# Optimization experiments

Hardware: AMD Instinct MI355X
Metric: run time of the kernel (lower is better)

The kernel has to match this reference:

```python
import jax, jax.numpy as jnp
import numpy as np

B, S, HID = 2, 2048, 2048
H, HKV, HD = 16, 4, 128  # heads, kv heads, head_dim; n_rep = H // HKV


def rotate_half(x):
    h = x.shape[-1] // 2
    return jnp.concatenate((-x[..., h:], x[..., :h]), axis=-1)


def setup_inputs() -> dict:
    key = jax.random.key(0)
    ks = jax.random.split(key, 7)
    sc = 0.02
    return {
        "x": jax.random.normal(ks[0], (B, S, HID), jnp.float32),
        "cos": jax.random.uniform(ks[1], (S, HD), jnp.float32),
        "sin": jax.random.uniform(ks[2], (S, HD), jnp.float32),
        "wq": jax.random.normal(ks[3], (H * HD, HID), jnp.float32) * sc,
        "wk": jax.random.normal(ks[4], (HKV * HD, HID), jnp.float32) * sc,
        "wv": jax.random.normal(ks[5], (HKV * HD, HID), jnp.float32) * sc,
        "wo": jax.random.normal(ks[6], (HID, H * HD), jnp.float32) * sc,
    }


def reference(x, cos, sin, wq, wk, wv, wo):
    bs, seq_len, _ = x.shape
    n_rep = H // HKV

    # projections (Linear with weight [out, in]: y = x @ W.T)
    q = (x @ wq.T).reshape(bs, seq_len, H, HD)
    k = (x @ wk.T).reshape(bs, seq_len, HKV, HD)
    v = (x @ wv.T).reshape(bs, seq_len, HKV, HD)

    # RoPE: cos/sin [S, HD] -> broadcast over heads (unsqueeze_dim=1 after seq)
    c = cos[:seq_len][:, None, :]  # [S,1,HD]
    s = sin[:seq_len][:, None, :]
    q = q * c + rotate_half(q) * s
    k = k * c + rotate_half(k) * s

    # repeat KV heads (GQA) and move heads forward: [b,h,s,d]
    k = jnp.repeat(k, n_rep, axis=2).transpose(0, 2, 1, 3)
    v = jnp.repeat(v, n_rep, axis=2).transpose(0, 2, 1, 3)
    q = q.transpose(0, 2, 1, 3)

    # causal SDPA
    scale = 1.0 / jnp.sqrt(jnp.float32(HD))
    scores = jnp.einsum("bhqd,bhkd->bhqk", q, k) * scale
    causal = jnp.tril(jnp.ones((seq_len, seq_len), bool))
    scores = jnp.where(causal, scores, jnp.float32(-jnp.inf))
    probs = jax.nn.softmax(scores, axis=-1)
    out = jnp.einsum("bhqk,bhkd->bhqd", probs, v)

    out = out.transpose(0, 2, 1, 3).reshape(bs, seq_len, H * HD)
    return out @ wo.T
```

## Files before the change

kernel.cpp:

```cpp
#include <hip/hip_runtime.h>
#include <hip/hip_bf16.h>
#include <math.h>

#define B_    2
#define S_    2048
#define HID_  2048
#define H_    16
#define HKV_  4
#define HD_   128
#define BS_   (B_*S_)
#define QSTRIDE 3072
#define L2E 1.4426950408889634f

typedef __attribute__((ext_vector_type(8))) short bf16x8;
typedef __attribute__((ext_vector_type(4))) float f32x4;
typedef __attribute__((ext_vector_type(16))) float f32x16;
typedef unsigned int uint;

typedef __attribute__((address_space(3))) void lds_void;
typedef __attribute__((address_space(1))) const void gbl_cvoid;

__device__ __forceinline__ void load_lds16(const void* g, void* l) {
  __builtin_amdgcn_global_load_lds((gbl_cvoid*)g, (lds_void*)l, 16, 0, 0);
}

__device__ __forceinline__ unsigned short f2bf(float f) {
  uint u = __float_as_uint(f);
  u = (u + 0x7fff + ((u >> 16) & 1)) >> 16;
  return (unsigned short)u;
}
__device__ __forceinline__ float bf2f(unsigned short u) {
  return __uint_as_float(((uint)u) << 16);
}
__device__ __forceinline__ uint cvtpk_bf16(float lo, float hi) {
  uint r;
  asm("v_cvt_pk_bf16_f32 %0, %1, %2" : "=v"(r) : "v"(lo), "v"(hi));
  return r;
}
__device__ __forceinline__ void swap32(uint& a, uint& b) {
  asm("v_permlane32_swap_b32 %0, %1" : "+v"(a), "+v"(b));
}

__global__ __launch_bounds__(256) void cast_f32_bf16(
    const float* __restrict__ src, unsigned short* __restrict__ dst, int n)
{
  int i = (blockIdx.x * 256 + threadIdx.x) * 4;
  if (i < n) {
    float4 v = *(const float4*)(src + i);
    ushort4 o;
    o.x = f2bf(v.x); o.y = f2bf(v.y); o.z = f2bf(v.z); o.w = f2bf(v.w);
    *(ushort4*)(dst + i) = o;
  }
}

template <int WRITE_BF16>
__global__ __launch_bounds__(256) void gemm_nt_bf16(
    const unsigned short* __restrict__ A, const unsigned short* __restrict__ W,
    void* __restrict__ Cv, int M, int N, int K)
{
  __shared__ unsigned short As[128 * 32];
  __shared__ unsigned short Bs[128 * 32];

  const int tid = threadIdx.x;
  const int bm = blockIdx.y * 128, bn = blockIdx.x * 128;
  const int w = tid >> 6, lane = tid & 63;
  const int c_ = lane & 15, g4 = lane >> 4;
  const int wr = (w >> 1) * 64, wc = (w & 1) * 64;

  f32x4 acc[4][4];
#pragma unroll
  for (int i = 0; i < 4; ++i)
#pragma unroll
    for (int j = 0; j < 4; ++j) acc[i][j] = (f32x4){0.f, 0.f, 0.f, 0.f};

  for (int k0 = 0; k0 < K; k0 += 32) {
#pragma unroll
    for (int i = 0; i < 2; ++i) {
      int db = i * 4096 + tid * 16;
      int row = db >> 6;
      int cb = (db & 63) ^ ((row & 3) << 4);
      load_lds16((const char*)(A + (size_t)(bm + row) * K + k0) + cb, (char*)As + db);
      load_lds16((const char*)(W + (size_t)(bn + row) * K + k0) + cb, (char*)Bs + db);
    }
    __syncthreads();

    bf16x8 af[4], bfr[4];
#pragma unroll
    for (int i = 0; i < 4; ++i) {
      int ra = wr + i * 16 + c_;
      af[i] = *(const bf16x8*)((const char*)As + ra * 64 + ((g4 * 16) ^ ((ra & 3) << 4)));
      int rb = wc + i * 16 + c_;
      bfr[i] = *(const bf16x8*)((const char*)Bs + rb * 64 + ((g4 * 16) ^ ((rb & 3) << 4)));
    }
#pragma unroll
    for (int mi = 0; mi < 4; ++mi)
#pragma unroll
      for (int ni = 0; ni < 4; ++ni)
        acc[mi][ni] = __builtin_amdgcn_mfma_f32_16x16x32_bf16(af[mi], bfr[ni], acc[mi][ni], 0, 0, 0);
    __syncthreads();
  }

#pragma unroll
  for (int mi = 0; mi < 4; ++mi) {
#pragma unroll
    for (int r = 0; r < 4; ++r) {
      size_t row = bm + wr + mi * 16 + g4 * 4 + r;
#pragma unroll
      for (int ni = 0; ni < 4; ++ni) {
        size_t col = bn + wc + ni * 16 + c_;
        float v = acc[mi][ni][r];
        if (WRITE_BF16)
          ((unsigned short*)Cv)[row * N + col] = f2bf(v);
        else
          ((float*)Cv)[row * N + col] = v;
      }
    }
  }
}

template <int NH, int LOGNH, int ROWE, int SCALE>
__global__ __launch_bounds__(256) void rope_bf16(
    unsigned short* __restrict__ p, const float* __restrict__ cosb,
    const float* __restrict__ sinb)
{
  int idx = blockIdx.x * 256 + threadIdx.x;
  int d = idx & 63;
  int h = (idx >> 6) & (NH - 1);
  int s = (idx >> (6 + LOGNH)) & (S_ - 1);
  int b = idx >> (6 + LOGNH + 11);

  size_t off = ((size_t)b * S_ + s) * ROWE + h * HD_ + d;
  float x1 = bf2f(p[off]);
  float x2 = bf2f(p[off + 64]);
  float c1 = cosb[s * HD_ + d],      s1 = sinb[s * HD_ + d];
  float c2 = cosb[s * HD_ + d + 64], s2 = sinb[s * HD_ + d + 64];
  float o1 = x1 * c1 - x2 * s1;
  float o2 = x2 * c2 + x1 * s2;
  if (SCALE) { o1 *= 0.08838834764831845f; o2 *= 0.08838834764831845f; }
  p[off]      = f2bf(o1);
  p[off + 64] = f2bf(o2);
}

__global__ __launch_bounds__(256) void attn_fwd_bf16(
    const unsigned short* __restrict__ QKV, unsigned short* __restrict__ O)
{
  __shared__ __align__(16) char lds[65536];

  const int tid = threadIdx.x;
  const int lane = tid & 63;
  const int wq = tid >> 6;
  const int ql = lane & 31;
  const int hi = lane >> 5;

  const int bid = blockIdx.x;
  const int halfg = bid >> 8, rem = bid & 255;
  const int bh = rem >> 3, a2 = rem & 7;
  const int qt = halfg ? (15 - 2 * a2) : (2 * a2);
  const int b = bh >> 4, h = bh & 15, kh = h >> 2;
  const int q0 = qt * 128;
  const int qglob = q0 + wq * 32 + ql;
  const int ktmax_w = (q0 + wq * 32 + 31) >> 6;
  const int ntiles = 2 * qt + 2;

  bf16x8 qf[8];
  {
    const unsigned short* qsrc =
        QKV + ((size_t)(b * S_) + qglob) * QSTRIDE + h * HD_ + hi * 8;
#pragma unroll
    for (int ds = 0; ds < 8; ++ds) qf[ds] = *(const bf16x8*)(qsrc + ds * 16);
  }

  f32x16 acc[4];
#pragma unroll
  for (int dt = 0; dt < 4; ++dt)
#pragma unroll
    for (int r = 0; r < 16; ++r) acc[dt][r] = 0.f;
  float m_ = -3.0e38f, l_ = 0.f;

  const char* Kg = (const char*)(QKV + (size_t)b * S_ * QSTRIDE + 2048 + kh * HD_);
  const unsigned short* Vg = QKV + (size_t)b * S_ * QSTRIDE + 2560 + kh * HD_;

  const int dc = tid & 15;
  const int kq4 = (tid >> 4) * 4;
  bf16x8 vr[4];

#pragma unroll
  for (int p = 0; p < 4; ++p) {
    int db = p * 4096 + tid * 16;
    int row = db >> 8;
    int cb = (db & 255) ^ ((row & 7) << 4);
    load_lds16(Kg + (size_t)row * (QSTRIDE * 2) + cb, lds + db);
  }
  {
    const unsigned short* vs = Vg + (size_t)kq4 * QSTRIDE + dc * 8;
#pragma unroll
    for (int i = 0; i < 4; ++i) vr[i] = *(const bf16x8*)(vs + i * QSTRIDE);
#pragma unroll
    for (int s = 0; s < 8; ++s) {
      int j = (dc + s) & 7;
      int d = dc * 8 + j;
      uint w0 = (uint)(unsigned short)vr[0][j] | ((uint)(unsigned short)vr[1][j] << 16);
      uint w1 = (uint)(unsigned short)vr[2][j] | ((uint)(unsigned short)vr[3][j] << 16);
      *(uint2*)(lds + 32768 + d * 128 + ((kq4 * 2) ^ (j << 4))) = make_uint2(w0, w1);
    }
  }
  __syncthreads();

  for (int kt = 0; kt < ntiles; ++kt) {
    const int cur = kt & 1;
    const bool pf = (kt + 1 < ntiles);

    if (pf) {
#pragma unroll
      for (int p = 0; p < 4; ++p) {
        int db = p * 4096 + tid * 16;
        int row = db >> 8;
        int cb = (db & 255) ^ ((row & 7) << 4);
        load_lds16(Kg + (size_t)((kt + 1) * 64 + row) * (QSTRIDE * 2) + cb,
                   lds + (cur ^ 1) * 16384 + db);
      }
      const unsigned short* vs = Vg + (size_t)((kt + 1) * 64 + kq4) * QSTRIDE + dc * 8;
#pragma unroll
      for (int i = 0; i < 4; ++i) vr[i] = *(const bf16x8*)(vs + i * QSTRIDE);
    }

    if (kt <= ktmax_w) {
      const char* ksc = lds + cur * 16384;
      const char* vtc = lds + 32768 + cur * 16384;
#pragma unroll
      for (int ks2 = 0; ks2 < 2; ++ks2) {
        f32x16 s;
#pragma unroll
        for (int r = 0; r < 16; ++r) s[r] = 0.f;
        const int kk = ks2 * 32 + ql;
        const char* krow = ksc + kk * 256;
        const int ksw = (kk & 7) << 4;
#pragma unroll
        for (int ds = 0; ds < 8; ++ds) {
          bf16x8 kf = *(const bf16x8*)(krow + ((ds * 32 + hi * 16) ^ ksw));
          s = __builtin_amdgcn_mfma_f32_32x32x16_bf16(kf, qf[ds], s, 0, 0, 0);
        }

        if (kt == ktmax_w) {
          const int kb = kt * 64 + ks2 * 32 + 4 * hi;
#pragma unroll
          for (int r = 0; r < 16; ++r) {
            int kg = kb + (r & 3) + 8 * (r >> 2);
            if (kg > qglob) s[r] = -3.0e38f;
          }
        }

        float mx = s[0];
#pragma unroll
        for (int r = 1; r < 16; ++r) mx = fmaxf(mx, s[r]);
        mx = fmaxf(mx, __shfl_xor(mx, 32));
        const bool nd = mx > m_ + 8.f;
        float fr = 1.f;
        if (__any(nd)) {
          float mn = nd ? mx : m_;
          fr = nd ? exp2f((m_ - mn) * L2E) : 1.f;
          m_ = mn;
#pragma unroll
          for (int dt = 0; dt < 4; ++dt)
#pragma unroll
            for (int r = 0; r < 16; ++r) acc[dt][r] *= fr;
        }
        float pr[16];
        float sum = 0.f;
#pragma unroll
        for (int r = 0; r < 16; ++r) {
          pr[r] = exp2f((s[r] - m_) * L2E);
          sum += pr[r];
        }
        sum += __shfl_xor(sum, 32);
        l_ = l_ * fr + sum;

        uint wA0 = cvtpk_bf16(pr[0], pr[1]);
        uint wA1 = cvtpk_bf16(pr[2], pr[3]);
        uint wB0 = cvtpk_bf16(pr[4], pr[5]);
        uint wB1 = cvtpk_bf16(pr[6], pr[7]);
        swap32(wA0, wB0);
        swap32(wA1, wB1);
        uint wC0 = cvtpk_bf16(pr[8], pr[9]);
        uint wC1 = cvtpk_bf16(pr[10], pr[11]);
        uint wD0 = cvtpk_bf16(pr[12], pr[13]);
        uint wD1 = cvtpk_bf16(pr[14], pr[15]);
        swap32(wC0, wD0);
        swap32(wC1, wD1);
        union { uint u[4]; bf16x8 v; } p0, p1;
        p0.u[0] = wA0; p0.u[1] = wA1; p0.u[2] = wB0; p0.u[3] = wB1;
        p1.u[0] = wC0; p1.u[1] = wC1; p1.u[2] = wD0; p1.u[3] = wD1;

#pragma unroll
        for (int dt = 0; dt < 4; ++dt) {
          const int dr = dt * 32 + ql;
          const char* vrow = vtc + dr * 128;
          const int vsw = (dr & 7) << 4;
          bf16x8 v0 = *(const bf16x8*)(vrow + ((ks2 * 64 + hi * 16) ^ vsw));
          acc[dt] = __builtin_amdgcn_mfma_f32_32x32x16_bf16(v0, p0.v, acc[dt], 0, 0, 0);
          bf16x8 v1 = *(const bf16x8*)(vrow + ((ks2 * 64 + 32 + hi * 16) ^ vsw));
          acc[dt] = __builtin_amdgcn_mfma_f32_32x32x16_bf16(v1, p1.v, acc[dt], 0, 0, 0);
        }
      }
    }

    if (pf) {
#pragma unroll
      for (int s = 0; s < 8; ++s) {
        int j = (dc + s) & 7;
        int d = dc * 8 + j;
        uint w0 = (uint)(unsigned short)vr[0][j] | ((uint)(unsigned short)vr[1][j] << 16);
        uint w1 = (uint)(unsigned short)vr[2][j] | ((uint)(unsigned short)vr[3][j] << 16);
        *(uint2*)(lds + 32768 + (cur ^ 1) * 16384 + d * 128 + ((kq4 * 2) ^ (j << 4))) =
            make_uint2(w0, w1);
      }
    }
    __syncthreads();
  }

  {
    const float inv = 1.f / l_;
    char* wsc = lds + wq * 8704;
#pragma unroll
    for (int dt = 0; dt < 4; ++dt) {
#pragma unroll
      for (int i = 0; i < 8; ++i) {
        uint wv = cvtpk_bf16(acc[dt][2 * i] * inv, acc[dt][2 * i + 1] * inv);
        int d = 2 * (i & 1) + 8 * (i >> 1) + 4 * hi + 32 * dt;
        *(uint*)(wsc + ql * 272 + d * 2) = wv;
      }
    }
#pragma unroll
    for (int j = 0; j < 8; ++j) {
      bf16x8 ov = *(const bf16x8*)(wsc + ql * 272 + hi * 128 + j * 16);
      unsigned short* ob = O + ((size_t)(b * S_) + q0 + wq * 32 + ql) * (H_ * HD_) +
                           h * HD_ + hi * 64 + j * 8;
      *(bf16x8*)ob = ov;
    }
  }
}

extern "C" void kernel_launch(void* const* d_in, const int* in_sizes, int n_in,
                              void* d_out, int out_size, void* d_ws, size_t ws_size,
                              hipStream_t stream) {
  const float* x    = (const float*)d_in[0];
  const float* cosb = (const float*)d_in[1];
  const float* sinb = (const float*)d_in[2];
  const float* wq   = (const float*)d_in[3];
  const float* wk   = (const float*)d_in[4];
  const float* wv   = (const float*)d_in[5];
  const float* wo   = (const float*)d_in[6];
  float* out        = (float*)d_out;

  unsigned short* xb     = (unsigned short*)d_ws;
  unsigned short* wqkvb  = xb + 8388608;
  unsigned short* wob    = wqkvb + 6291456;
  unsigned short* qkv    = wob + 4194304;
  unsigned short* attnb  = qkv + 12582912;

  dim3 blk(256);

  cast_f32_bf16<<<8192, blk, 0, stream>>>(x, xb, 8388608);
  cast_f32_bf16<<<4096, blk, 0, stream>>>(wq, wqkvb, 4194304);
  cast_f32_bf16<<<1024, blk, 0, stream>>>(wk, wqkvb + 4194304, 1048576);
  cast_f32_bf16<<<1024, blk, 0, stream>>>(wv, wqkvb + 5242880, 1048576);
  cast_f32_bf16<<<4096, blk, 0, stream>>>(wo, wob, 4194304);

  gemm_nt_bf16<1><<<dim3(24, 32), blk, 0, stream>>>(xb, wqkvb, qkv, BS_, QSTRIDE, HID_);

  rope_bf16<16, 4, QSTRIDE, 1><<<16384, blk, 0, stream>>>(qkv, cosb, sinb);
  rope_bf16<4, 2, QSTRIDE, 0><<<4096, blk, 0, stream>>>(qkv + 2048, cosb, sinb);

  attn_fwd_bf16<<<512, blk, 0, stream>>>(qkv, attnb);

  gemm_nt_bf16<0><<<dim3(16, 32), blk, 0, stream>>>(attnb, wob, out, BS_, HID_, HID_);
}
```

Before: 379.1 us.

## Replace GEMM with 8-wave double-buffered 256-row tile pipeline

Replaces the simple 128x128 single-buffered bf16 GEMM with a 512-thread kernel using 256xBN tiles, a 64-wide K step split into two slabs, and double-buffered LDS. Global-to-LDS loads for the next tile are interleaved between MFMA phases, with explicit vmcnt waits and raised wave priority around the MFMA blocks. The goal is to hide memory latency and raise data reuse for the QKV and output projections. In exchange it uses much more LDS and registers, and the fewer, larger tiles may leave some compute units underused.

Measured after the change: 345.4 us. -8.9%, faster.

```diff
diff --git a/kernel.cpp b/kernel.cpp
--- a/kernel.cpp
+++ b/kernel.cpp
@@ -53,69 +53,159 @@
   }
 }
 
-template <int WRITE_BF16>
-__global__ __launch_bounds__(256) void gemm_nt_bf16(
+template <int BN, int WRITE_BF16>
+__global__ __launch_bounds__(512, 2) void gemm_nt_8ph(
     const unsigned short* __restrict__ A, const unsigned short* __restrict__ W,
     void* __restrict__ Cv, int M, int N, int K)
 {
-  __shared__ unsigned short As[128 * 32];
-  __shared__ unsigned short Bs[128 * 32];
+  constexpr int ASLAB = 16384;
+  constexpr int BSLAB = BN * 64;
+  constexpr int ABUF  = 2 * ASLAB;
+  constexpr int BBUF  = 2 * BSLAB;
+  constexpr int RN    = BN / 4;
+  constexpr int NTN   = RN / 16;
+
+  __shared__ __align__(16) char lds_[2 * ABUF + 2 * BBUF];
+  char* const AL = lds_;
+  char* const BL = lds_ + 2 * ABUF;
 
   const int tid = threadIdx.x;
-  const int bm = blockIdx.y * 128, bn = blockIdx.x * 128;
-  const int w = tid >> 6, lane = tid & 63;
+  const int lane = tid & 63;
+  const int wid = tid >> 6;
+  const int wm = wid >> 2, wn = wid & 3;
   const int c_ = lane & 15, g4 = lane >> 4;
-  const int wr = (w >> 1) * 64, wc = (w & 1) * 64;
-
-  f32x4 acc[4][4];
-#pragma unroll
-  for (int i = 0; i < 4; ++i)
-#pragma unroll
-    for (int j = 0; j < 4; ++j) acc[i][j] = (f32x4){0.f, 0.f, 0.f, 0.f};
-
-  for (int k0 = 0; k0 < K; k0 += 32) {
-#pragma unroll
-    for (int i = 0; i < 2; ++i) {
-      int db = i * 4096 + tid * 16;
-      int row = db >> 6;
-      int cb = (db & 63) ^ ((row & 3) << 4);
-      load_lds16((const char*)(A + (size_t)(bm + row) * K + k0) + cb, (char*)As + db);
-      load_lds16((const char*)(W + (size_t)(bn + row) * K + k0) + cb, (char*)Bs + db);
-    }
-    __syncthreads();
-
-    bf16x8 af[4], bfr[4];
-#pragma unroll
-    for (int i = 0; i < 4; ++i) {
-      int ra = wr + i * 16 + c_;
-      af[i] = *(const bf16x8*)((const char*)As + ra * 64 + ((g4 * 16) ^ ((ra & 3) << 4)));
-      int rb = wc + i * 16 + c_;
-      bfr[i] = *(const bf16x8*)((const char*)Bs + rb * 64 + ((g4 * 16) ^ ((rb & 3) << 4)));
-    }
-#pragma unroll
-    for (int mi = 0; mi < 4; ++mi)
-#pragma unroll
-      for (int ni = 0; ni < 4; ++ni)
-        acc[mi][ni] = __builtin_amdgcn_mfma_f32_16x16x32_bf16(af[mi], bfr[ni], acc[mi][ni], 0, 0, 0);
-    __syncthreads();
-  }
-
-#pragma unroll
-  for (int mi = 0; mi < 4; ++mi) {
-#pragma unroll
-    for (int r = 0; r < 4; ++r) {
-      size_t row = bm + wr + mi * 16 + g4 * 4 + r;
-#pragma unroll
-      for (int ni = 0; ni < 4; ++ni) {
-        size_t col = bn + wc + ni * 16 + c_;
-        float v = acc[mi][ni][r];
-        if (WRITE_BF16)
-          ((unsigned short*)Cv)[row * N + col] = f2bf(v);
-        else
-          ((float*)Cv)[row * N + col] = v;
+  const int bm = blockIdx.y * 256, bn = blockIdx.x * BN;
+
+  const size_t rs = (size_t)K * 2;
+  const char* Ag = (const char*)A + (size_t)bm * rs;
+  const char* Bg = (const char*)W + (size_t)bn * rs;
+
+  const int stq = tid >> 2;
+  const int stslot = ((tid & 3) ^ (stq & 3)) * 16;
+  const int fsl = (g4 ^ (c_ & 3)) << 4;
+  const int dst = tid * 16;
+
+  f32x4 acc[2][4][NTN];
+#pragma unroll
+  for (int mh = 0; mh < 2; ++mh)
+#pragma unroll
+    for (int mt = 0; mt < 4; ++mt)
+#pragma unroll
+      for (int nt = 0; nt < NTN; ++nt) acc[mh][mt][nt] = (f32x4){0.f, 0.f, 0.f, 0.f};
+
+  const int NT = K / 64;
+
+  auto stA = [&](char* buf, int slab, int half, int kbyte) {
+    load_lds16(Ag + (size_t)(half * 128 + stq) * rs + kbyte + stslot,
+               buf + slab * ASLAB + half * 8192 + dst);
+  };
+  auto stB = [&](char* buf, int slab, int half, int kbyte) {
+    load_lds16(Bg + (size_t)(half * 128 + stq) * rs + kbyte + stslot,
+               buf + slab * BSLAB + half * 8192 + dst);
+  };
+
+  stA(AL, 0, 0, 0); stB(BL, 0, 0, 0); stA(AL, 0, 1, 0);
+  if constexpr (BN == 256) stB(BL, 0, 1, 0);
+  stA(AL, 1, 0, 64); stB(BL, 1, 0, 64); stA(AL, 1, 1, 64);
+  if constexpr (BN == 256) stB(BL, 1, 1, 64);
+
+  const int afb = (wm * 128 + c_) * 64 + fsl;
+  const int bfb = (wn * RN + c_) * 64 + fsl;
+
+#define WAITK do { if constexpr (BN == 256) asm volatile("s_waitcnt vmcnt(4)" ::: "memory"); \
+                   else                     asm volatile("s_waitcnt vmcnt(3)" ::: "memory"); \
+                   __builtin_amdgcn_s_barrier(); \
+                   __builtin_amdgcn_sched_barrier(0); } while (0)
+
+  for (int t = 0; t < NT; ++t) {
+    const char* Ac = AL + (t & 1) * ABUF;
+    const char* Bc = BL + (t & 1) * BBUF;
+    char* An = AL + ((t + 1) & 1) * ABUF;
+    char* Bn = BL + ((t + 1) & 1) * BBUF;
+    const int tn = (t + 1 < NT) ? t + 1 : 0;
+    const int kb = tn * 128;
+
+    WAITK;
+
+    bf16x8 af[4], bf0[NTN];
+
+#pragma unroll
+    for (int mt = 0; mt < 4; ++mt)
+      af[mt] = *(const bf16x8*)(Ac + afb + mt * 1024);
+#pragma unroll
+    for (int nt = 0; nt < NTN; ++nt)
+      bf0[nt] = *(const bf16x8*)(Bc + bfb + nt * 1024);
+    stA(An, 0, 0, kb); stB(Bn, 0, 0, kb);
+    __builtin_amdgcn_s_setprio(1);
+#pragma unroll
+    for (int mt = 0; mt < 4; ++mt)
+#pragma unroll
+      for (int nt = 0; nt < NTN; ++nt)
+        acc[0][mt][nt] = __builtin_amdgcn_mfma_f32_16x16x32_bf16(af[mt], bf0[nt], acc[0][mt][nt], 0, 0, 0);
+    __builtin_amdgcn_s_setprio(0);
+
+#pragma unroll
+    for (int mt = 0; mt < 4; ++mt)
+      af[mt] = *(const bf16x8*)(Ac + afb + 4096 + mt * 1024);
+    stA(An, 0, 1, kb);
+    if constexpr (BN == 256) stB(Bn, 0, 1, kb);
+    __builtin_amdgcn_s_setprio(1);
+#pragma unroll
+    for (int mt = 0; mt < 4; ++mt)
+#pragma unroll
+      for (int nt = 0; nt < NTN; ++nt)
+        acc[1][mt][nt] = __builtin_amdgcn_mfma_f32_16x16x32_bf16(af[mt], bf0[nt], acc[1][mt][nt], 0, 0, 0);
+    __builtin_amdgcn_s_setprio(0);
+
+    WAITK;
+
+#pragma unroll
+    for (int mt = 0; mt < 4; ++mt)
+      af[mt] = *(const bf16x8*)(Ac + ASLAB + afb + mt * 1024);
+#pragma unroll
+    for (int nt = 0; nt < NTN; ++nt)
+      bf0[nt] = *(const bf16x8*)(Bc + BSLAB + bfb + nt * 1024);
+    stA(An, 1, 0, kb + 64); stB(Bn, 1, 0, kb + 64);
+    __builtin_amdgcn_s_setprio(1);
+#pragma unroll
+    for (int mt = 0; mt < 4; ++mt)
+#pragma unroll
+      for (int nt = 0; nt < NTN; ++nt)
+        acc[0][mt][nt] = __builtin_amdgcn_mfma_f32_16x16x32_bf16(af[mt], bf0[nt], acc[0][mt][nt], 0, 0, 0);
+    __builtin_amdgcn_s_setprio(0);
+
+#pragma unroll
+    for (int mt = 0; mt < 4; ++mt)
+      af[mt] = *(const bf16x8*)(Ac + ASLAB + afb + 4096 + mt * 1024);
+    stA(An, 1, 1, kb + 64);
+    if constexpr (BN == 256) stB(Bn, 1, 1, kb + 64);
+    __builtin_amdgcn_s_setprio(1);
+#pragma unroll
+    for (int mt = 0; mt < 4; ++mt)
+#pragma unroll
+      for (int nt = 0; nt < NTN; ++nt)
+        acc[1][mt][nt] = __builtin_amdgcn_mfma_f32_16x16x32_bf16(af[mt], bf0[nt], acc[1][mt][nt], 0, 0, 0);
+    __builtin_amdgcn_s_setprio(0);
+  }
+#undef WAITK
+
+#pragma unroll
+  for (int mh = 0; mh < 2; ++mh)
+#pragma unroll
+    for (int mt = 0; mt < 4; ++mt)
+#pragma unroll
+      for (int r = 0; r < 4; ++r) {
+        size_t row = bm + wm * 128 + mh * 64 + mt * 16 + g4 * 4 + r;
+#pragma unroll
+        for (int nt = 0; nt < NTN; ++nt) {
+          size_t col = bn + wn * RN + nt * 16 + c_;
+          float v = acc[mh][mt][nt][r];
+          if (WRITE_BF16)
+            ((unsigned short*)Cv)[row * N + col] = f2bf(v);
+          else
+            ((float*)Cv)[row * N + col] = v;
+        }
       }
-    }
-  }
 }
 
 template <int NH, int LOGNH, int ROWE, int SCALE>
@@ -366,12 +456,14 @@
   cast_f32_bf16<<<1024, blk, 0, stream>>>(wv, wqkvb + 5242880, 1048576);
   cast_f32_bf16<<<4096, blk, 0, stream>>>(wo, wob, 4194304);
 
-  gemm_nt_bf16<1><<<dim3(24, 32), blk, 0, stream>>>(xb, wqkvb, qkv, BS_, QSTRIDE, HID_);
+  gemm_nt_8ph<256, 1><<<dim3(12, 16), dim3(512), 0, stream>>>(
+      xb, wqkvb, qkv, BS_, QSTRIDE, HID_);
 
   rope_bf16<16, 4, QSTRIDE, 1><<<16384, blk, 0, stream>>>(qkv, cosb, sinb);
   rope_bf16<4, 2, QSTRIDE, 0><<<4096, blk, 0, stream>>>(qkv + 2048, cosb, sinb);
 
   attn_fwd_bf16<<<512, blk, 0, stream>>>(qkv, attnb);
 
-  gemm_nt_bf16<0><<<dim3(16, 32), blk, 0, stream>>>(attnb, wob, out, BS_, HID_, HID_);
-}
+  gemm_nt_8ph<128, 0><<<dim3(16, 16), dim3(512), 0, stream>>>(
+      attnb, wob, out, BS_, HID_, HID_);
+}
```
